# Kernel optimization log

Measured on AMD Instinct MI355X. Metric: run time of the kernel, lower is better.

The kernel has to match this reference:

```python
import jax, jax.numpy as jnp
import numpy as np

TEMPERATURE = 2.5  # TopKRouter temperature from MoELayer.__init__
TOPK = 2


def setup_inputs() -> dict:
    key = jax.random.key(0)
    ks = jax.random.split(key, 4)
    B, T, D, F, E = 8, 8192, 512, 2048, 8
    x = jax.random.normal(ks[0], (B, T, D), jnp.float32)
    Wr = jax.random.normal(ks[1], (D, E), jnp.float32) * (D ** -0.5)
    W1 = jax.random.normal(ks[2], (E, D, F), jnp.float32) * (D ** -0.5)
    b1 = jnp.zeros((E, F), jnp.float32)
    W2 = jax.random.normal(ks[3], (E, F, D), jnp.float32) * (F ** -0.5)
    b2 = jnp.zeros((E, D), jnp.float32)
    return {"x": x, "Wr": Wr, "W1": W1, "b1": b1, "W2": W2, "b2": b2}


def reference(x, Wr, W1, b1, W2, b2):
    # x: (B, T, D); eval-mode MoE: no router noise, no capacity, no dropout.
    B, T, D = x.shape
    E = Wr.shape[1]
    N = B * T
    xf = x.reshape(N, D)

    # Router: softmax(logits / temperature), then top-k, renormalize kept probs.
    logits = xf @ Wr                                  # (N, E)
    probs = jax.nn.softmax(logits / TEMPERATURE, axis=-1)
    topk_vals, topk_idx = jax.lax.top_k(probs, TOPK)  # (N, K)
    topk_vals = topk_vals / jnp.sum(topk_vals, axis=-1, keepdims=True)

    # Scatter top-k weights into per-expert combine weights w: (N, E).
    w = jnp.zeros((N, E), xf.dtype)
    w = w.at[jnp.arange(N)[:, None], topk_idx].add(topk_vals)

    # Weighted combine of expert FFN outputs (fixed small loop over E experts).
    out = jnp.zeros_like(xf)
    for e in range(E):
        h = jax.nn.gelu(xf @ W1[e] + b1[e])           # (N, F)
        out = out + w[:, e:e + 1] * (h @ W2[e] + b2[e])
    return out.reshape(B, T, D)
```

## Files before the change

kernel.cpp:

```cpp
#include <hip/hip_runtime.h>
#include <cstdint>
#include <cstddef>

#define N_TOK 65536
#define DIM 512
#define FF 2048
#define NE 8
#define HCAP 24576
#define MAXT 1032

typedef __attribute__((ext_vector_type(8))) short short8;
typedef __attribute__((ext_vector_type(4))) float f32x4;

__device__ __forceinline__ unsigned f2bf(float f) {
  unsigned u = __builtin_bit_cast(unsigned, f);
  u = u + 0x7fffu + ((u >> 16) & 1u);
  return (u >> 16) & 0xffffu;
}

__device__ __forceinline__ void gload_lds16(const void* g, void* l) {
  __builtin_amdgcn_global_load_lds((const __attribute__((address_space(1))) void*)g,
                                   (__attribute__((address_space(3))) void*)l, 16, 0, 0);
}

__global__ __launch_bounds__(256) void k_transpose_cast(
    const float* __restrict__ in, unsigned short* __restrict__ outp, int rows, int cols)
{
  __shared__ float tile[32][33];
  const float* ine = in + (size_t)blockIdx.z * rows * cols;
  unsigned short* oute = outp + (size_t)blockIdx.z * rows * cols;
  int tx = threadIdx.x & 31, ty = threadIdx.x >> 5;
  int r0 = blockIdx.y * 32, c0 = blockIdx.x * 32;
#pragma unroll
  for (int i = 0; i < 4; ++i)
    tile[ty + i*8][tx] = ine[(size_t)(r0 + ty + i*8)*cols + c0 + tx];
  __syncthreads();
#pragma unroll
  for (int i = 0; i < 4; ++i) {
    int r = c0 + ty + i*8, c = r0 + tx;
    oute[(size_t)r*rows + c] = (unsigned short)f2bf(tile[tx][ty + i*8]);
  }
}

__global__ __launch_bounds__(256) void k_router(
    const float* __restrict__ x, const float* __restrict__ Wr,
    unsigned short* __restrict__ xb, int2* __restrict__ tinfo, int* __restrict__ cnt)
{
  __shared__ int lcnt[8];
  int tid = threadIdx.x, lane = tid & 63, wv = tid >> 6;
  if (tid < 8) lcnt[tid] = 0;
  float wr[8][8];
#pragma unroll
  for (int j = 0; j < 8; ++j) {
    const float4* p = (const float4*)(Wr + (size_t)(lane*8 + j)*NE);
    float4 a = p[0], b = p[1];
    wr[j][0]=a.x; wr[j][1]=a.y; wr[j][2]=a.z; wr[j][3]=a.w;
    wr[j][4]=b.x; wr[j][5]=b.y; wr[j][6]=b.z; wr[j][7]=b.w;
  }
  __syncthreads();
  int t0 = blockIdx.x*64 + wv*16;
  for (int it = 0; it < 16; ++it) {
    int t = t0 + it;
    const float4* xp = (const float4*)(x + (size_t)t*DIM + lane*8);
    float4 v0 = xp[0], v1 = xp[1];
    float xv[8] = {v0.x,v0.y,v0.z,v0.w,v1.x,v1.y,v1.z,v1.w};
    uint4 pk;
    pk.x = f2bf(xv[0]) | (f2bf(xv[1]) << 16);
    pk.y = f2bf(xv[2]) | (f2bf(xv[3]) << 16);
    pk.z = f2bf(xv[4]) | (f2bf(xv[5]) << 16);
    pk.w = f2bf(xv[6]) | (f2bf(xv[7]) << 16);
    *(uint4*)(xb + (size_t)t*DIM + lane*8) = pk;
    float lg[8];
#pragma unroll
    for (int e2 = 0; e2 < 8; ++e2) lg[e2] = 0.f;
#pragma unroll
    for (int j = 0; j < 8; ++j)
#pragma unroll
      for (int e2 = 0; e2 < 8; ++e2) lg[e2] += xv[j]*wr[j][e2];
#pragma unroll
    for (int off = 32; off >= 1; off >>= 1)
#pragma unroll
      for (int e2 = 0; e2 < 8; ++e2) lg[e2] += __shfl_xor(lg[e2], off, 64);
    int e0 = 0; float v0m = lg[0];
#pragma unroll
    for (int e2 = 1; e2 < 8; ++e2) if (lg[e2] > v0m) { v0m = lg[e2]; e0 = e2; }
    int e1 = -1; float v1m = -3.0e38f;
#pragma unroll
    for (int e2 = 0; e2 < 8; ++e2) if (e2 != e0 && lg[e2] > v1m) { v1m = lg[e2]; e1 = e2; }
    float w0 = 1.f / (1.f + __expf((v1m - v0m) * 0.4f));
    if (lane == 0) {
      atomicAdd(&lcnt[e0], 1);
      atomicAdd(&lcnt[e1], 1);
      tinfo[t] = make_int2(e0 | (e1 << 8), __float_as_int(w0));
    }
  }
  __syncthreads();
  if (tid < 8) atomicAdd(&cnt[tid*16], lcnt[tid]);
}

__global__ void k_offsets(int* cnt) {
  if (threadIdx.x == 0) {
    int base = 0, tb = 0;
    for (int e2 = 0; e2 < 8; ++e2) {
      int c = cnt[e2*16]; if (c > HCAP) c = HCAP;
      cnt[e2*16 + 1] = base;
      base += cnt[e2*16];
      cnt[e2*16 + 2] = 0;
      cnt[e2*16 + 3] = tb;
      tb += (c + 127) >> 7;
    }
    cnt[135] = tb;
  }
}

__global__ __launch_bounds__(128) void k_fill(
    const int2* __restrict__ tinfo, int* __restrict__ tokl,
    float* __restrict__ pwl, int* __restrict__ cnt)
{
  __shared__ int lc[8], lbase[8], gb[8];
  __shared__ unsigned char ce[128];
  __shared__ int csl[128];
  __shared__ float cw[128];
  int tid = threadIdx.x;
  if (tid < 8) { lc[tid] = 0; gb[tid] = cnt[tid*16 + 1]; }
  __syncthreads();
  if (tid < 64) {
    int t = blockIdx.x*64 + tid;
    int2 inf = tinfo[t];
    int e0 = inf.x & 0xff, e1 = (inf.x >> 8) & 0xff;
    float w0 = __int_as_float(inf.y);
    int i0 = tid*2, i1 = i0 + 1;
    ce[i0] = (unsigned char)e0; cw[i0] = w0;        csl[i0] = atomicAdd(&lc[e0], 1);
    ce[i1] = (unsigned char)e1; cw[i1] = 1.f - w0;  csl[i1] = atomicAdd(&lc[e1], 1);
  }
  __syncthreads();
  if (tid < 8) lbase[tid] = atomicAdd(&cnt[tid*16 + 2], lc[tid]);
  __syncthreads();
  int e = ce[tid];
  int p = gb[e] + lbase[e] + csl[tid];
  tokl[p] = blockIdx.x*64 + (tid >> 1);
  pwl[p]  = cw[tid];
}

__device__ __forceinline__ void stage128(
    const unsigned short* __restrict__ src, size_t stride, int k0,
    unsigned short* __restrict__ buf, int tid)
{
#pragma unroll
  for (int j = 0; j < 4; ++j) {
    int lrow = j*32 + (tid >> 3);
    gload_lds16(src + (size_t)lrow*stride + k0 + (((tid & 7) ^ (lrow & 7)) << 3),
                buf + j*2048 + tid*8);
  }
}

__device__ __forceinline__ int tile_expert(const int* cnt, int gt) {
  int e = 0;
#pragma unroll
  for (int k = 1; k < 8; ++k) if (gt >= cnt[k*16 + 3]) e = k;
  return e;
}

__global__ __launch_bounds__(256, 2) void k_gemm1(
    const unsigned short* __restrict__ xb, const unsigned short* __restrict__ w1t,
    const float* __restrict__ b1, const int* __restrict__ cnt,
    const int* __restrict__ tokl, unsigned short* __restrict__ h, int T0, int cap)
{
  const int bid = blockIdx.x;
  const int n  = (bid & 7) | (((bid >> 3) & 1) << 3);
  const int lt = bid >> 4;
  const int gt = T0 + lt;
  if (lt >= cap || gt >= cnt[135]) return;
  const int e = tile_expert(cnt, gt);
  const int m = gt - cnt[e*16 + 3];
  const int count0 = cnt[e*16];
  const int count = count0 < HCAP ? count0 : HCAP;
  const int row0 = m*128;
  const int gbase = cnt[e*16 + 1];

  __shared__ __align__(16) unsigned short lds[32768];
  unsigned short* As = lds;
  unsigned short* Bs = lds + 16384;

  const int tid = threadIdx.x, lane = tid & 63, wv = tid >> 6;
  const int r16 = lane & 15, g4 = lane >> 4;
  const int wm = wv >> 1, wn = wv & 1;

  int rows4[4];
#pragma unroll
  for (int j = 0; j < 4; ++j) {
    int rr = row0 + j*32 + (tid >> 3);
    if (rr > count - 1) rr = count - 1;
    rows4[j] = tokl[gbase + rr];
  }
  const int axor = ((tid & 7) ^ ((tid >> 3) & 7)) << 3;
  const unsigned short* w1p = w1t + (size_t)e*FF*DIM + (size_t)(n*128)*DIM;

  auto stageA = [&](unsigned short* buf, int k0) {
#pragma unroll
    for (int j = 0; j < 4; ++j)
      gload_lds16(xb + (size_t)rows4[j]*DIM + k0 + axor, buf + j*2048 + tid*8);
  };

  const f32x4 fz = {0.f, 0.f, 0.f, 0.f};
  f32x4 acc[4][4];
#pragma unroll
  for (int a = 0; a < 4; ++a)
#pragma unroll
    for (int b = 0; b < 4; ++b) acc[a][b] = fz;

  stageA(As, 0);
  stage128(w1p, DIM, 0, Bs, tid);
  __syncthreads();
  int buf = 0;
  for (int kk = 0; kk < DIM/64; ++kk) {
    if (kk + 1 < DIM/64) {
      stageA(As + (buf ^ 1)*8192, (kk + 1)*64);
      stage128(w1p, DIM, (kk + 1)*64, Bs + (buf ^ 1)*8192, tid);
    }
    const unsigned short* ab = As + buf*8192;
    const unsigned short* bb = Bs + buf*8192;
    short8 af[4][2], bf[4][2];
#pragma unroll
    for (int mf = 0; mf < 4; ++mf) {
      int row = wm*64 + mf*16 + r16;
#pragma unroll
      for (int k2 = 0; k2 < 2; ++k2)
        af[mf][k2] = *(const short8*)(ab + row*64 + ((((k2 << 2) + g4) ^ (row & 7)) << 3));
    }
#pragma unroll
    for (int nf = 0; nf < 4; ++nf) {
      int row = wn*64 + nf*16 + r16;
#pragma unroll
      for (int k2 = 0; k2 < 2; ++k2)
        bf[nf][k2] = *(const short8*)(bb + row*64 + ((((k2 << 2) + g4) ^ (row & 7)) << 3));
    }
    __builtin_amdgcn_s_setprio(1);
#pragma unroll
    for (int k2 = 0; k2 < 2; ++k2)
#pragma unroll
      for (int mf = 0; mf < 4; ++mf)
#pragma unroll
        for (int nf = 0; nf < 4; ++nf)
          acc[mf][nf] = __builtin_amdgcn_mfma_f32_16x16x32_bf16(
              af[mf][k2], bf[nf][k2], acc[mf][nf], 0, 0, 0);
    __builtin_amdgcn_s_setprio(0);
    __syncthreads();
    buf ^= 1;
  }

  float b1v[4];
#pragma unroll
  for (int nf = 0; nf < 4; ++nf)
    b1v[nf] = b1[(size_t)e*FF + n*128 + wn*64 + nf*16 + r16];

  unsigned short* hs = lds;
#pragma unroll
  for (int mf = 0; mf < 4; ++mf)
#pragma unroll
    for (int nf = 0; nf < 4; ++nf) {
      int col = wn*64 + nf*16 + r16;
#pragma unroll
      for (int i = 0; i < 4; ++i) {
        int row = wm*64 + mf*16 + g4*4 + i;
        float v = acc[mf][nf][i] + b1v[nf];
        float u = 0.7978845608028654f * (v + 0.044715f*v*v*v);
        float gl = v / (1.f + __expf(-2.f*u));
        hs[row*136 + col] = (unsigned short)f2bf(gl);
      }
    }
  __syncthreads();
  unsigned short* hdst = h + (size_t)lt*(128*FF);
#pragma unroll
  for (int j = 0; j < 8; ++j) {
    int o = j*256 + tid;
    int row = o >> 4, part = o & 15;
    if (row0 + row < count)
      *(uint4*)(hdst + (size_t)row*FF + n*128 + part*8) =
          *(const uint4*)(hs + row*136 + part*8);
  }
}

__global__ __launch_bounds__(256, 2) void k_gemm2(
    const unsigned short* __restrict__ h, const unsigned short* __restrict__ w2t,
    const float* __restrict__ b2, const int* __restrict__ tokl,
    const float* __restrict__ pwl, const int* __restrict__ cnt,
    float* __restrict__ out, int T0, int cap)
{
  const int bid = blockIdx.x;
  const int lt = (bid >> 5)*8 + (bid & 7);
  const int n  = (bid >> 3) & 3;
  const int gt = T0 + lt;
  if (lt >= cap || gt >= cnt[135]) return;
  const int e = tile_expert(cnt, gt);
  const int m = gt - cnt[e*16 + 3];
  const int count0 = cnt[e*16];
  const int count = count0 < HCAP ? count0 : HCAP;
  const int row0 = m*128;
  const int gbase = cnt[e*16 + 1];

  __shared__ __align__(16) unsigned short lds[32768];
  unsigned short* As = lds;
  unsigned short* Bs = lds + 16384;

  const int tid = threadIdx.x, lane = tid & 63, wv = tid >> 6;
  const int r16 = lane & 15, g4 = lane >> 4;
  const int wm = wv >> 1, wn = wv & 1;

  const unsigned short* ap = h + (size_t)lt*(128*FF);
  const unsigned short* bp = w2t + (size_t)e*DIM*FF + (size_t)(n*128)*FF;

  const f32x4 fz = {0.f, 0.f, 0.f, 0.f};
  f32x4 acc[4][4];
#pragma unroll
  for (int a = 0; a < 4; ++a)
#pragma unroll
    for (int b = 0; b < 4; ++b) acc[a][b] = fz;

  stage128(ap, FF, 0, As, tid);
  stage128(bp, FF, 0, Bs, tid);
  __syncthreads();
  int buf = 0;
  for (int kk = 0; kk < FF/64; ++kk) {
    if (kk + 1 < FF/64) {
      stage128(ap, FF, (kk + 1)*64, As + (buf ^ 1)*8192, tid);
      stage128(bp, FF, (kk + 1)*64, Bs + (buf ^ 1)*8192, tid);
    }
    const unsigned short* ab = As + buf*8192;
    const unsigned short* bb = Bs + buf*8192;
    short8 af[4][2], bf[4][2];
#pragma unroll
    for (int mf = 0; mf < 4; ++mf) {
      int row = wm*64 + mf*16 + r16;
#pragma unroll
      for (int k2 = 0; k2 < 2; ++k2)
        af[mf][k2] = *(const short8*)(ab + row*64 + ((((k2 << 2) + g4) ^ (row & 7)) << 3));
    }
#pragma unroll
    for (int nf = 0; nf < 4; ++nf) {
      int row = wn*64 + nf*16 + r16;
#pragma unroll
      for (int k2 = 0; k2 < 2; ++k2)
        bf[nf][k2] = *(const short8*)(bb + row*64 + ((((k2 << 2) + g4) ^ (row & 7)) << 3));
    }
    __builtin_amdgcn_s_setprio(1);
#pragma unroll
    for (int k2 = 0; k2 < 2; ++k2)
#pragma unroll
      for (int mf = 0; mf < 4; ++mf)
#pragma unroll
        for (int nf = 0; nf < 4; ++nf)
          acc[mf][nf] = __builtin_amdgcn_mfma_f32_16x16x32_bf16(
              af[mf][k2], bf[nf][k2], acc[mf][nf], 0, 0, 0);
    __builtin_amdgcn_s_setprio(0);
    __syncthreads();
    buf ^= 1;
  }

  float b2v[4];
#pragma unroll
  for (int nf = 0; nf < 4; ++nf)
    b2v[nf] = b2[(size_t)e*DIM + n*128 + wn*64 + nf*16 + r16];

#pragma unroll
  for (int mf = 0; mf < 4; ++mf)
#pragma unroll
    for (int i = 0; i < 4; ++i) {
      int lrow = row0 + wm*64 + mf*16 + g4*4 + i;
      if (lrow < count) {
        int tk = tokl[gbase + lrow];
        float wg = pwl[gbase + lrow];
#pragma unroll
        for (int nf = 0; nf < 4; ++nf) {
          int d = n*128 + wn*64 + nf*16 + r16;
          atomicAdd(out + (size_t)tk*DIM + d, (acc[mf][nf][i] + b2v[nf]) * wg);
        }
      }
    }
}

extern "C" void kernel_launch(void* const* d_in, const int* in_sizes, int n_in,
                              void* d_out, int out_size, void* d_ws, size_t ws_size,
                              hipStream_t stream)
{
  const float* x  = (const float*)d_in[0];
  const float* Wr = (const float*)d_in[1];
  const float* W1 = (const float*)d_in[2];
  const float* b1 = (const float*)d_in[3];
  const float* W2 = (const float*)d_in[4];
  const float* b2 = (const float*)d_in[5];
  float* out = (float*)d_out;
  (void)in_sizes; (void)n_in;

  char* ws = (char*)d_ws;
  unsigned short* xb  = (unsigned short*)(ws);
  unsigned short* w1t = (unsigned short*)(ws + 67108864);
  unsigned short* w2t = (unsigned short*)(ws + 83886080);
  int2*  tinfo = (int2*)(ws + 100663296);
  int*   tokl  = (int*)(ws + 101187584);
  float* pwl   = (float*)(ws + 101711872);
  int*   cnt   = (int*)(ws + 102236160);
  unsigned short* h = (unsigned short*)(ws + 102237184);

  const size_t FIXED = 102237184ULL;
  const size_t TILEB = (size_t)128 * FF * 2;
  long cap_l = (ws_size > FIXED) ? (long)((ws_size - FIXED) / TILEB) : 0;
  int cap = (int)(cap_l < MAXT ? cap_l : MAXT);
  if (cap > 256) cap = 256;
  if (cap < 8)  cap = 8;
  const int nch = (MAXT + cap - 1) / cap;
  const int ngrp = (cap + 7) / 8;

  hipMemsetAsync(cnt, 0, 256*sizeof(int), stream);
  hipMemsetAsync(d_out, 0, (size_t)out_size*sizeof(float), stream);

  dim3 g1(FF/32, DIM/32, NE);
  k_transpose_cast<<<g1, 256, 0, stream>>>(W1, w1t, DIM, FF);
  dim3 g2(DIM/32, FF/32, NE);
  k_transpose_cast<<<g2, 256, 0, stream>>>(W2, w2t, FF, DIM);

  k_router<<<N_TOK/64, 256, 0, stream>>>(x, Wr, xb, tinfo, cnt);
  k_offsets<<<1, 64, 0, stream>>>(cnt);
  k_fill<<<N_TOK/64, 128, 0, stream>>>(tinfo, tokl, pwl, cnt);

  for (int c = 0; c < nch; ++c) {
    const int T0 = c * cap;
    k_gemm1<<<ngrp*128, 256, 0, stream>>>(xb, w1t, b1, cnt, tokl, h, T0, cap);
    k_gemm2<<<ngrp*32,  256, 0, stream>>>(h, w2t, b2, tokl, pwl, cnt, out, T0, cap);
  }
}
```

Before: 1.181 ms.

## Single-buffer LDS in both expert GEMMs to raise occupancy to four blocks

Drops the double-buffered LDS pipeline in both expert GEMM kernels, halving shared memory per block to 32 KB, and raises launch bounds to four blocks per CU. The GELU epilogue now stages its output in two column halves so it fits in the smaller LDS. The intent is to hide global-load latency through more resident waves instead of intra-block prefetch. In exchange, loads and MFMAs within a block no longer overlap, each iteration carries an extra barrier, and the tighter register budget may cause spills.

```diff
diff --git a/kernel.cpp b/kernel.cpp
--- a/kernel.cpp
+++ b/kernel.cpp
@@ -161,7 +161,38 @@
   return e;
 }
 
-__global__ __launch_bounds__(256, 2) void k_gemm1(
+__device__ __forceinline__ void mfma_step(
+    const unsigned short* __restrict__ ab, const unsigned short* __restrict__ bb,
+    f32x4 acc[4][4], int r16, int g4, int wm, int wn)
+{
+  short8 af[4][2], bf[4][2];
+#pragma unroll
+  for (int mf = 0; mf < 4; ++mf) {
+    int row = wm*64 + mf*16 + r16;
+#pragma unroll
+    for (int k2 = 0; k2 < 2; ++k2)
+      af[mf][k2] = *(const short8*)(ab + row*64 + ((((k2 << 2) + g4) ^ (row & 7)) << 3));
+  }
+#pragma unroll
+  for (int nf = 0; nf < 4; ++nf) {
+    int row = wn*64 + nf*16 + r16;
+#pragma unroll
+    for (int k2 = 0; k2 < 2; ++k2)
+      bf[nf][k2] = *(const short8*)(bb + row*64 + ((((k2 << 2) + g4) ^ (row & 7)) << 3));
+  }
+  __builtin_amdgcn_s_setprio(1);
+#pragma unroll
+  for (int k2 = 0; k2 < 2; ++k2)
+#pragma unroll
+    for (int mf = 0; mf < 4; ++mf)
+#pragma unroll
+      for (int nf = 0; nf < 4; ++nf)
+        acc[mf][nf] = __builtin_amdgcn_mfma_f32_16x16x32_bf16(
+            af[mf][k2], bf[nf][k2], acc[mf][nf], 0, 0, 0);
+  __builtin_amdgcn_s_setprio(0);
+}
+
+__global__ __launch_bounds__(256, 4) void k_gemm1(
     const unsigned short* __restrict__ xb, const unsigned short* __restrict__ w1t,
     const float* __restrict__ b1, const int* __restrict__ cnt,
     const int* __restrict__ tokl, unsigned short* __restrict__ h, int T0, int cap)
@@ -178,9 +209,9 @@
   const int row0 = m*128;
   const int gbase = cnt[e*16 + 1];
 
-  __shared__ __align__(16) unsigned short lds[32768];
+  __shared__ __align__(16) unsigned short lds[16384];
   unsigned short* As = lds;
-  unsigned short* Bs = lds + 16384;
+  unsigned short* Bs = lds + 8192;
 
   const int tid = threadIdx.x, lane = tid & 63, wv = tid >> 6;
   const int r16 = lane & 15, g4 = lane >> 4;
@@ -196,12 +227,6 @@
   const int axor = ((tid & 7) ^ ((tid >> 3) & 7)) << 3;
   const unsigned short* w1p = w1t + (size_t)e*FF*DIM + (size_t)(n*128)*DIM;
 
-  auto stageA = [&](unsigned short* buf, int k0) {
-#pragma unroll
-    for (int j = 0; j < 4; ++j)
-      gload_lds16(xb + (size_t)rows4[j]*DIM + k0 + axor, buf + j*2048 + tid*8);
-  };
-
   const f32x4 fz = {0.f, 0.f, 0.f, 0.f};
   f32x4 acc[4][4];
 #pragma unroll
@@ -209,44 +234,14 @@
 #pragma unroll
     for (int b = 0; b < 4; ++b) acc[a][b] = fz;
 
-  stageA(As, 0);
-  stage128(w1p, DIM, 0, Bs, tid);
-  __syncthreads();
-  int buf = 0;
   for (int kk = 0; kk < DIM/64; ++kk) {
-    if (kk + 1 < DIM/64) {
-      stageA(As + (buf ^ 1)*8192, (kk + 1)*64);
-      stage128(w1p, DIM, (kk + 1)*64, Bs + (buf ^ 1)*8192, tid);
-    }
-    const unsigned short* ab = As + buf*8192;
-    const unsigned short* bb = Bs + buf*8192;
-    short8 af[4][2], bf[4][2];
-#pragma unroll
-    for (int mf = 0; mf < 4; ++mf) {
-      int row = wm*64 + mf*16 + r16;
-#pragma unroll
-      for (int k2 = 0; k2 < 2; ++k2)
-        af[mf][k2] = *(const short8*)(ab + row*64 + ((((k2 << 2) + g4) ^ (row & 7)) << 3));
-    }
-#pragma unroll
-    for (int nf = 0; nf < 4; ++nf) {
-      int row = wn*64 + nf*16 + r16;
-#pragma unroll
-      for (int k2 = 0; k2 < 2; ++k2)
-        bf[nf][k2] = *(const short8*)(bb + row*64 + ((((k2 << 2) + g4) ^ (row & 7)) << 3));
-    }
-    __builtin_amdgcn_s_setprio(1);
-#pragma unroll
-    for (int k2 = 0; k2 < 2; ++k2)
-#pragma unroll
-      for (int mf = 0; mf < 4; ++mf)
-#pragma unroll
-        for (int nf = 0; nf < 4; ++nf)
-          acc[mf][nf] = __builtin_amdgcn_mfma_f32_16x16x32_bf16(
-              af[mf][k2], bf[nf][k2], acc[mf][nf], 0, 0, 0);
-    __builtin_amdgcn_s_setprio(0);
-    __syncthreads();
-    buf ^= 1;
+#pragma unroll
+    for (int j = 0; j < 4; ++j)
+      gload_lds16(xb + (size_t)rows4[j]*DIM + kk*64 + axor, As + j*2048 + tid*8);
+    stage128(w1p, DIM, kk*64, Bs, tid);
+    __syncthreads();
+    mfma_step(As, Bs, acc, r16, g4, wm, wn);
+    __syncthreads();
   }
 
   float b1v[4];
@@ -255,33 +250,39 @@
     b1v[nf] = b1[(size_t)e*FF + n*128 + wn*64 + nf*16 + r16];
 
   unsigned short* hs = lds;
-#pragma unroll
-  for (int mf = 0; mf < 4; ++mf)
-#pragma unroll
-    for (int nf = 0; nf < 4; ++nf) {
-      int col = wn*64 + nf*16 + r16;
-#pragma unroll
-      for (int i = 0; i < 4; ++i) {
-        int row = wm*64 + mf*16 + g4*4 + i;
-        float v = acc[mf][nf][i] + b1v[nf];
-        float u = 0.7978845608028654f * (v + 0.044715f*v*v*v);
-        float gl = v / (1.f + __expf(-2.f*u));
-        hs[row*136 + col] = (unsigned short)f2bf(gl);
-      }
+  unsigned short* hdst = h + (size_t)lt*(128*FF);
+#pragma unroll
+  for (int half = 0; half < 2; ++half) {
+    if (wn == half) {
+#pragma unroll
+      for (int mf = 0; mf < 4; ++mf)
+#pragma unroll
+        for (int nf = 0; nf < 4; ++nf) {
+          int lcol = nf*16 + r16;
+#pragma unroll
+          for (int i = 0; i < 4; ++i) {
+            int row = wm*64 + mf*16 + g4*4 + i;
+            float v = acc[mf][nf][i] + b1v[nf];
+            float u = 0.7978845608028654f * (v + 0.044715f*v*v*v);
+            float gl = v / (1.f + __expf(-2.f*u));
+            hs[row*68 + lcol] = (unsigned short)f2bf(gl);
+          }
+        }
     }
-  __syncthreads();
-  unsigned short* hdst = h + (size_t)lt*(128*FF);
-#pragma unroll
-  for (int j = 0; j < 8; ++j) {
-    int o = j*256 + tid;
-    int row = o >> 4, part = o & 15;
-    if (row0 + row < count)
-      *(uint4*)(hdst + (size_t)row*FF + n*128 + part*8) =
-          *(const uint4*)(hs + row*136 + part*8);
-  }
-}
-
-__global__ __launch_bounds__(256, 2) void k_gemm2(
+    __syncthreads();
+#pragma unroll
+    for (int j = 0; j < 4; ++j) {
+      int o = j*256 + tid;
+      int row = o >> 3, part = o & 7;
+      if (row0 + row < count)
+        *(uint4*)(hdst + (size_t)row*FF + n*128 + half*64 + part*8) =
+            *(const uint4*)(hs + row*68 + part*8);
+    }
+    __syncthreads();
+  }
+}
+
+__global__ __launch_bounds__(256, 4) void k_gemm2(
     const unsigned short* __restrict__ h, const unsigned short* __restrict__ w2t,
     const float* __restrict__ b2, const int* __restrict__ tokl,
     const float* __restrict__ pwl, const int* __restrict__ cnt,
@@ -299,9 +300,9 @@
   const int row0 = m*128;
   const int gbase = cnt[e*16 + 1];
 
-  __shared__ __align__(16) unsigned short lds[32768];
+  __shared__ __align__(16) unsigned short lds[16384];
   unsigned short* As = lds;
-  unsigned short* Bs = lds + 16384;
+  unsigned short* Bs = lds + 8192;
 
   const int tid = threadIdx.x, lane = tid & 63, wv = tid >> 6;
   const int r16 = lane & 15, g4 = lane >> 4;
@@ -317,44 +318,12 @@
 #pragma unroll
     for (int b = 0; b < 4; ++b) acc[a][b] = fz;
 
-  stage128(ap, FF, 0, As, tid);
-  stage128(bp, FF, 0, Bs, tid);
-  __syncthreads();
-  int buf = 0;
   for (int kk = 0; kk < FF/64; ++kk) {
-    if (kk + 1 < FF/64) {
-      stage128(ap, FF, (kk + 1)*64, As + (buf ^ 1)*8192, tid);
-      stage128(bp, FF, (kk + 1)*64, Bs + (buf ^ 1)*8192, tid);
-    }
-    const unsigned short* ab = As + buf*8192;
-    const unsigned short* bb = Bs + buf*8192;
-    short8 af[4][2], bf[4][2];
-#pragma unroll
-    for (int mf = 0; mf < 4; ++mf) {
-      int row = wm*64 + mf*16 + r16;
-#pragma unroll
-      for (int k2 = 0; k2 < 2; ++k2)
-        af[mf][k2] = *(const short8*)(ab + row*64 + ((((k2 << 2) + g4) ^ (row & 7)) << 3));
-    }
-#pragma unroll
-    for (int nf = 0; nf < 4; ++nf) {
-      int row = wn*64 + nf*16 + r16;
-#pragma unroll
-      for (int k2 = 0; k2 < 2; ++k2)
-        bf[nf][k2] = *(const short8*)(bb + row*64 + ((((k2 << 2) + g4) ^ (row & 7)) << 3));
-    }
-    __builtin_amdgcn_s_setprio(1);
-#pragma unroll
-    for (int k2 = 0; k2 < 2; ++k2)
-#pragma unroll
-      for (int mf = 0; mf < 4; ++mf)
-#pragma unroll
-        for (int nf = 0; nf < 4; ++nf)
-          acc[mf][nf] = __builtin_amdgcn_mfma_f32_16x16x32_bf16(
-              af[mf][k2], bf[nf][k2], acc[mf][nf], 0, 0, 0);
-    __builtin_amdgcn_s_setprio(0);
-    __syncthreads();
-    buf ^= 1;
+    stage128(ap, FF, kk*64, As, tid);
+    stage128(bp, FF, kk*64, Bs, tid);
+    __syncthreads();
+    mfma_step(As, Bs, acc, r16, g4, wm, wn);
+    __syncthreads();
   }
 
   float b2v[4];
```

Result: slower. 1.693 ms (+43.3%).
